# Kernel optimization log

Measured on AMD Instinct MI355X. Metric: run time of the kernel, lower is better.

## Reference

```python
import jax, jax.numpy as jnp
import numpy as np
import math

B, C, L = 16, 2048, 64

def setup_inputs() -> dict:
    key = jax.random.key(0)
    kq, kk, kv = jax.random.split(key, 3)
    q = jax.random.normal(kq, (B, C, L), dtype=jnp.float32)
    k = jax.random.normal(kk, (B, C, L), dtype=jnp.float32)
    v = jax.random.normal(kv, (B, C, L), dtype=jnp.float32)
    return {"q": q, "k": k, "v": v}

def reference(q, k, v):
    b, c, l = q.shape
    # Faithful to the torch source: k is RESHAPED (row-major), not transposed.
    k_t = k.reshape(b, l, c)                      # (b, l, c)
    score = jnp.matmul(q, k_t) / math.sqrt(l)     # (b, c, c)
    # nn.Softmax() with no dim on a 3D tensor -> torch implicit dim = 0 (batch axis)
    score = jax.nn.softmax(score, axis=0)
    return jnp.matmul(score, v)                   # (b, c, l)
```

## Files before the change

kernel.cpp:

```cpp
#include <hip/hip_runtime.h>

typedef __attribute__((ext_vector_type(8))) short short8;
typedef __attribute__((ext_vector_type(4))) float float4v;

#define BATCH 16
#define CDIM 2048
#define LDIM 64
#define BSTRIDE (CDIM * LDIM)

#if __has_builtin(__builtin_amdgcn_exp2f)
#define EXPW(x) __builtin_amdgcn_exp2f(x)
#define QSCALE 0.18033688011112042f
#else
#define EXPW(x) __expf(x)
#define QSCALE 0.125f
#endif

#define WAITV(n) asm volatile("s_waitcnt vmcnt(" #n ")" ::: "memory")
#define BARRIER() asm volatile("s_barrier" ::: "memory")

__device__ __forceinline__ float bf2f(unsigned short u) {
    return __uint_as_float(((unsigned int)u) << 16);
}
__device__ __forceinline__ unsigned short f2bf(float f) {
    unsigned int x = __float_as_uint(f);
    x += 0x7fffu + ((x >> 16) & 1u);
    return (unsigned short)(x >> 16);
}
#if __has_builtin(__builtin_amdgcn_cvt_pk_bf16_f32)
__device__ __forceinline__ unsigned int pk2bf(float a, float b) {
    auto t = __builtin_amdgcn_cvt_pk_bf16_f32(a, b);
    unsigned int u;
    __builtin_memcpy(&u, &t, 4);
    return u;
}
#else
__device__ __forceinline__ unsigned int pk2bf(float a, float b) {
    return f2bf(a) | ((unsigned)f2bf(b) << 16);
}
#endif
__device__ __forceinline__ void dma16(const void* g, void* l) {
    __builtin_amdgcn_global_load_lds(
        (const __attribute__((address_space(1))) void*)g,
        (__attribute__((address_space(3))) void*)l, 16, 0, 0);
}

__global__ __launch_bounds__(256) void prepass_kernel(
    const float* __restrict__ q, const float* __restrict__ k,
    unsigned short* __restrict__ qb, unsigned short* __restrict__ kT)
{
    __shared__ float T[64][68];
    const int bx = blockIdx.x;
    const int t = threadIdx.x;

    if (bx < 1024) {
        int i = bx * 256 + t;
        const float4v* src = (const float4v*)q + (size_t)i * 2;
        float4v x0 = src[0], x1 = src[1];
        unsigned int u0 = pk2bf(x0[0] * QSCALE, x0[1] * QSCALE);
        unsigned int u1 = pk2bf(x0[2] * QSCALE, x0[3] * QSCALE);
        unsigned int u2 = pk2bf(x1[0] * QSCALE, x1[1] * QSCALE);
        unsigned int u3 = pk2bf(x1[2] * QSCALE, x1[3] * QSCALE);
        int b = i >> 14, r = i & 16383, m = r >> 3, j = r & 7;
        *(uint4*)(qb + (size_t)b * BSTRIDE + m * 64 + (j ^ (m & 7)) * 8) =
            make_uint4(u0, u1, u2, u3);
    } else {
        int idx = bx - 1024, b = idx >> 5, n0 = (idx & 31) * 64;
        const float* src = k + (size_t)b * BSTRIDE + (size_t)(t >> 2) * 2048 + n0 + (t & 3) * 16;
#pragma unroll
        for (int kk = 0; kk < 4; kk++) {
            float4v x = *(const float4v*)(src + kk * 4);
#pragma unroll
            for (int e = 0; e < 4; e++)
                T[t >> 2][(t & 3) * 16 + kk * 4 + e] = x[e];
        }
        __syncthreads();
        unsigned short* dst = kT + (size_t)b * BSTRIDE;
        int n = t & 63;
#pragma unroll
        for (int jj = 0; jj < 2; jj++) {
            int j = (t >> 6) * 2 + jj;
            *(uint4*)(dst + (size_t)(n0 + n) * 64 + (j ^ (n & 7)) * 8) =
                make_uint4(pk2bf(T[j * 8 + 0][n], T[j * 8 + 1][n]),
                           pk2bf(T[j * 8 + 2][n], T[j * 8 + 3][n]),
                           pk2bf(T[j * 8 + 4][n], T[j * 8 + 5][n]),
                           pk2bf(T[j * 8 + 6][n], T[j * 8 + 7][n]));
        }
    }
}

__global__ __launch_bounds__(256, 3) void dinv_vpre_kernel(
    const unsigned short* __restrict__ qb, const unsigned short* __restrict__ kT,
    const float* __restrict__ v, unsigned short* __restrict__ vS,
    unsigned short* __restrict__ Dt)
{
    __shared__ __align__(16) unsigned char smem[24576];

    const int tid = threadIdx.x;

    if (blockIdx.x >= 512) {
        float (*T)[68] = (float(*)[68])smem;
#pragma unroll 1
        for (int tt = 0; tt < 2; tt++) {
            int idx = (blockIdx.x - 512) * 2 + tt, b = idx >> 5, n0 = (idx & 31) * 64;
            const float* src = v + (size_t)b * BSTRIDE + (size_t)n0 * 64 +
                               (size_t)(tid >> 2) * 64 + (tid & 3) * 16;
#pragma unroll
            for (int kk = 0; kk < 4; kk++) {
                float4v x = *(const float4v*)(src + kk * 4);
#pragma unroll
                for (int e = 0; e < 4; e++)
                    T[tid >> 2][(tid & 3) * 16 + kk * 4 + e] = x[e];
            }
            __syncthreads();
            unsigned short* dst = vS + (size_t)b * BSTRIDE;
            int j = tid & 63, qc = tid >> 6;
            int sw = qc ^ (j & 3) ^ ((j >> 2) & 3);
#pragma unroll
            for (int nb = 0; nb < 2; nb++) {
                *(uint4*)(dst + (size_t)(n0 / 32 + nb) * 2048 + j * 32 + sw * 8) =
                    make_uint4(pk2bf(T[nb * 32 + qc * 8 + 0][j], T[nb * 32 + qc * 8 + 1][j]),
                               pk2bf(T[nb * 32 + qc * 8 + 2][j], T[nb * 32 + qc * 8 + 3][j]),
                               pk2bf(T[nb * 32 + qc * 8 + 4][j], T[nb * 32 + qc * 8 + 5][j]),
                               pk2bf(T[nb * 32 + qc * 8 + 6][j], T[nb * 32 + qc * 8 + 7][j]));
            }
            __syncthreads();
        }
        return;
    }

    const int w = tid >> 6, lane = tid & 63;
    const int c = lane & 15, q = lane >> 4;
    const int xcd = blockIdx.x & 7, slot = blockIdx.x >> 3;
    const int mtB = xcd * 2 + (slot >> 5), ng = slot & 31;
    const int m0 = mtB * 128, n0 = ng * 64;

    float4v Dacc[2][4];
#pragma unroll
    for (int ms = 0; ms < 2; ms++)
#pragma unroll
        for (int nt = 0; nt < 4; nt++) Dacc[ms][nt] = (float4v){0.f, 0.f, 0.f, 0.f};

    const char* qrow0 = (const char*)qb + (size_t)(m0 + w * 32 + c) * 128;
    short8 Qf[2][2], Qn[2][2];
#pragma unroll
    for (int ms = 0; ms < 2; ms++)
#pragma unroll
        for (int h = 0; h < 2; h++)
            Qf[ms][h] = *(const short8*)(qrow0 + ms * 16 * 128 + ((h * 4 + q) ^ (c & 7)) * 16);

    {
        const char* kg0 = (const char*)(kT + (size_t)n0 * 64);
        const char* kg1 = (const char*)(kT + (size_t)BSTRIDE + (size_t)n0 * 64);
        dma16(kg0 + (w * 2 + 0) * 1024 + lane * 16, (char*)smem + (w * 2 + 0) * 1024);
        dma16(kg0 + (w * 2 + 1) * 1024 + lane * 16, (char*)smem + (w * 2 + 1) * 1024);
        dma16(kg1 + (w * 2 + 0) * 1024 + lane * 16, (char*)smem + 8192 + (w * 2 + 0) * 1024);
        dma16(kg1 + (w * 2 + 1) * 1024 + lane * 16, (char*)smem + 8192 + (w * 2 + 1) * 1024);
    }

    int cur = 0, pre = 2;
    for (int bb = 0; bb < BATCH; bb++) {
        if (bb == 0) { WAITV(2); }
        else if (bb == 15) { WAITV(4); }
        else { WAITV(6); }
        BARRIER();

        if (bb < BATCH - 1) {
            const char* qn = qrow0 + (size_t)(bb + 1) * (BSTRIDE * 2);
#pragma unroll
            for (int ms = 0; ms < 2; ms++)
#pragma unroll
                for (int h = 0; h < 2; h++)
                    Qn[ms][h] = *(const short8*)(qn + ms * 16 * 128 + ((h * 4 + q) ^ (c & 7)) * 16);
        }
        if (bb < BATCH - 2) {
            const char* kg = (const char*)(kT + (size_t)(bb + 2) * BSTRIDE + (size_t)n0 * 64);
            dma16(kg + (w * 2 + 0) * 1024 + lane * 16,
                  (char*)smem + pre * 8192 + (w * 2 + 0) * 1024);
            dma16(kg + (w * 2 + 1) * 1024 + lane * 16,
                  (char*)smem + pre * 8192 + (w * 2 + 1) * 1024);
        }
        const char* sk = (const char*)smem + cur * 8192;
        __builtin_amdgcn_s_setprio(1);
#pragma unroll
        for (int nt = 0; nt < 4; nt++) {
            short8 A0 = *(const short8*)(sk + (nt * 16 + c) * 128 + ((q) ^ (c & 7)) * 16);
            short8 A1 = *(const short8*)(sk + (nt * 16 + c) * 128 + ((4 + q) ^ (c & 7)) * 16);
#pragma unroll
            for (int ms = 0; ms < 2; ms++) {
                float4v d = (float4v){0.f, 0.f, 0.f, 0.f};
                d = __builtin_amdgcn_mfma_f32_16x16x32_bf16(A0, Qf[ms][0], d, 0, 0, 0);
                d = __builtin_amdgcn_mfma_f32_16x16x32_bf16(A1, Qf[ms][1], d, 0, 0, 0);
#pragma unroll
                for (int r = 0; r < 4; r++) Dacc[ms][nt][r] += EXPW(d[r]);
            }
        }
        __builtin_amdgcn_s_setprio(0);
        if (bb < BATCH - 1) {
#pragma unroll
            for (int ms = 0; ms < 2; ms++)
#pragma unroll
                for (int h = 0; h < 2; h++)
                    Qf[ms][h] = Qn[ms][h];
        }
        cur = (cur == 2) ? 0 : cur + 1;
        pre = (pre == 2) ? 0 : pre + 1;
    }

#pragma unroll
    for (int ms = 0; ms < 2; ms++)
#pragma unroll
        for (int nt = 0; nt < 4; nt++) {
            unsigned int x = pk2bf(__builtin_amdgcn_rcpf(Dacc[ms][nt][0]),
                                   __builtin_amdgcn_rcpf(Dacc[ms][nt][1]));
            unsigned int y = pk2bf(__builtin_amdgcn_rcpf(Dacc[ms][nt][2]),
                                   __builtin_amdgcn_rcpf(Dacc[ms][nt][3]));
            size_t tm = (size_t)(mtB * 8 + w * 2 + ms);
            size_t tp = (size_t)(ng * 2 + (nt >> 1));
            *(uint2*)((char*)Dt + (tm * 64 + tp) * 1024 + c * 64 + q * 16 + (nt & 1) * 8) =
                make_uint2(x, y);
        }
}

__global__ __launch_bounds__(512, 4) void attn_main_kernel(
    const unsigned short* __restrict__ qb, const unsigned short* __restrict__ kT,
    const unsigned short* __restrict__ vS, const unsigned short* __restrict__ Dt,
    float* __restrict__ out)
{
    __shared__ __align__(16) unsigned char smem[49152];

    const int tid = threadIdx.x, w = tid >> 6, lane = tid & 63;
    const int c = lane & 15, q = lane >> 4;
    const int g = w >> 2, ns = w & 3;
    const int xcd = blockIdx.x & 7, slot = blockIdx.x >> 3;
    const int b = slot & 15, mt = xcd * 4 + (slot >> 4);
    const int m0 = mt * 64;
    const int nbase = ns * 512;

    const unsigned short* qb_b = qb + (size_t)b * BSTRIDE;
    const char* kbase = (const char*)(kT + (size_t)b * BSTRIDE);
    const char* vbase = (const char*)(vS + (size_t)b * BSTRIDE);
    char* skb = (char*)smem + ns * 12288;

    short8 Qf[2][2];
#pragma unroll
    for (int ms = 0; ms < 2; ms++)
#pragma unroll
        for (int h = 0; h < 2; h++)
            Qf[ms][h] = *(const short8*)(qb_b + (m0 + g * 32 + ms * 16 + c) * 64 +
                                         ((h * 4 + q) ^ (c & 7)) * 8);
    float4v acc[2][4];
#pragma unroll
    for (int ms = 0; ms < 2; ms++)
#pragma unroll
        for (int jt = 0; jt < 4; jt++) acc[ms][jt] = (float4v){0.f, 0.f, 0.f, 0.f};

    const char* dtw0 = (const char*)Dt +
        ((size_t)(mt * 4 + g * 2 + 0) * 64 + ns * 16) * 1024 + c * 64 + q * 16;
    const char* dtw1 = dtw0 + (size_t)64 * 1024;

    const int vsw = (q ^ (c & 3) ^ ((c >> 2) & 3)) * 16;

    dma16(kbase + (size_t)nbase * 128 + (2 * g + 0) * 1024 + lane * 16, skb + (2 * g + 0) * 1024);
    dma16(kbase + (size_t)nbase * 128 + (2 * g + 1) * 1024 + lane * 16, skb + (2 * g + 1) * 1024);
    dma16(kbase + (size_t)(nbase + 32) * 128 + (2 * g + 0) * 1024 + lane * 16,
          skb + 4096 + (2 * g + 0) * 1024);
    dma16(kbase + (size_t)(nbase + 32) * 128 + (2 * g + 1) * 1024 + lane * 16,
          skb + 4096 + (2 * g + 1) * 1024);
    uint4 du[2];
    du[0] = *(const uint4*)(dtw0);
    du[1] = *(const uint4*)(dtw1);

    int cur = 0, pre = 2;
    for (int st = 0; st < 16; st++) {
        if (st == 0) { WAITV(4); }
        else if (st == 15) { WAITV(0); }
        else { WAITV(8); }
        BARRIER();

        uint4 nu[2] = {du[0], du[1]};
        if (st < 15) {
            nu[0] = *(const uint4*)(dtw0 + (size_t)(st + 1) * 1024);
            nu[1] = *(const uint4*)(dtw1 + (size_t)(st + 1) * 1024);
        }
        short8 Vr[4];
        {
            const char* vtile = vbase + (size_t)(ns * 16 + st) * 4096;
#pragma unroll
            for (int jt = 0; jt < 4; jt++)
                Vr[jt] = *(const short8*)(vtile + (jt * 16 + c) * 64 + vsw);
        }
        if (st < 14) {
            const int n2 = nbase + (st + 2) * 32;
            dma16(kbase + (size_t)n2 * 128 + (2 * g + 0) * 1024 + lane * 16,
                  skb + pre * 4096 + (2 * g + 0) * 1024);
            dma16(kbase + (size_t)n2 * 128 + (2 * g + 1) * 1024 + lane * 16,
                  skb + pre * 4096 + (2 * g + 1) * 1024);
        }

        const char* skp = skb + cur * 4096;
        unsigned int pr[2][2][2];
        __builtin_amdgcn_s_setprio(1);
#pragma unroll
        for (int nt = 0; nt < 2; nt++) {
            short8 A0 = *(const short8*)(skp + (nt * 16 + c) * 128 + ((q) ^ (c & 7)) * 16);
            short8 A1 = *(const short8*)(skp + (nt * 16 + c) * 128 + ((4 + q) ^ (c & 7)) * 16);
#pragma unroll
            for (int ms = 0; ms < 2; ms++) {
                float4v d = (float4v){0.f, 0.f, 0.f, 0.f};
                d = __builtin_amdgcn_mfma_f32_16x16x32_bf16(A0, Qf[ms][0], d, 0, 0, 0);
                d = __builtin_amdgcn_mfma_f32_16x16x32_bf16(A1, Qf[ms][1], d, 0, 0, 0);
                unsigned int ux = nt ? du[ms].z : du[ms].x;
                unsigned int uy = nt ? du[ms].w : du[ms].y;
                pr[ms][nt][0] = pk2bf(EXPW(d[0]) * __uint_as_float(ux << 16),
                                      EXPW(d[1]) * __uint_as_float(ux & 0xffff0000u));
                pr[ms][nt][1] = pk2bf(EXPW(d[2]) * __uint_as_float(uy << 16),
                                      EXPW(d[3]) * __uint_as_float(uy & 0xffff0000u));
            }
        }
        __builtin_amdgcn_s_setprio(0);

        union PU { unsigned int i[4]; short8 s; };
        PU pu0, pu1;
#if __has_builtin(__builtin_amdgcn_permlane32_swap) && __has_builtin(__builtin_amdgcn_permlane16_swap)
        {
            typedef __attribute__((ext_vector_type(2))) unsigned int uint2v;
            uint2v ab, cd;
            ab = __builtin_amdgcn_permlane32_swap(pr[0][0][0], pr[0][1][0], false, false);
            cd = __builtin_amdgcn_permlane16_swap(ab.x, ab.y, false, false);
            pu0.i[0] = cd.x; pu0.i[2] = cd.y;
            ab = __builtin_amdgcn_permlane32_swap(pr[0][0][1], pr[0][1][1], false, false);
            cd = __builtin_amdgcn_permlane16_swap(ab.x, ab.y, false, false);
            pu0.i[1] = cd.x; pu0.i[3] = cd.y;
            ab = __builtin_amdgcn_permlane32_swap(pr[1][0][0], pr[1][1][0], false, false);
            cd = __builtin_amdgcn_permlane16_swap(ab.x, ab.y, false, false);
            pu1.i[0] = cd.x; pu1.i[2] = cd.y;
            ab = __builtin_amdgcn_permlane32_swap(pr[1][0][1], pr[1][1][1], false, false);
            cd = __builtin_amdgcn_permlane16_swap(ab.x, ab.y, false, false);
            pu1.i[1] = cd.x; pu1.i[3] = cd.y;
        }
#else
#pragma unroll
        for (int t = 0; t < 4; t++) {
            int src = (2 * (q & 1) + (t >> 1)) * 16 + c;
            int a0 = __shfl((int)pr[0][0][t & 1], src);
            int b0 = __shfl((int)pr[0][1][t & 1], src);
            pu0.i[t] = (unsigned int)((q >= 2) ? b0 : a0);
            int a1 = __shfl((int)pr[1][0][t & 1], src);
            int b1 = __shfl((int)pr[1][1][t & 1], src);
            pu1.i[t] = (unsigned int)((q >= 2) ? b1 : a1);
        }
#endif

        __builtin_amdgcn_s_setprio(1);
#pragma unroll
        for (int jt = 0; jt < 4; jt++) {
            acc[0][jt] = __builtin_amdgcn_mfma_f32_16x16x32_bf16(pu0.s, Vr[jt], acc[0][jt], 0, 0, 0);
            acc[1][jt] = __builtin_amdgcn_mfma_f32_16x16x32_bf16(pu1.s, Vr[jt], acc[1][jt], 0, 0, 0);
        }
        __builtin_amdgcn_s_setprio(0);
        du[0] = nu[0]; du[1] = nu[1];
        cur = (cur == 2) ? 0 : cur + 1;
        pre = (pre == 2) ? 0 : pre + 1;
    }

    __syncthreads();
    {
        float* cpy = (float*)((char*)smem + (ns & 1) * 17408);
        if (ns < 2) {
#pragma unroll
            for (int ms = 0; ms < 2; ms++)
#pragma unroll
                for (int jt = 0; jt < 4; jt++)
#pragma unroll
                    for (int r = 0; r < 4; r++)
                        cpy[(g * 32 + ms * 16 + q * 4 + r) * 68 + jt * 16 + c] = acc[ms][jt][r];
        }
    }
    __syncthreads();
    {
        float* cpy = (float*)((char*)smem + (ns & 1) * 17408);
        if (ns >= 2) {
#pragma unroll
            for (int ms = 0; ms < 2; ms++)
#pragma unroll
                for (int jt = 0; jt < 4; jt++)
#pragma unroll
                    for (int r = 0; r < 4; r++)
                        cpy[(g * 32 + ms * 16 + q * 4 + r) * 68 + jt * 16 + c] += acc[ms][jt][r];
        }
    }
    __syncthreads();
    {
        int ml = tid >> 3, j0 = (tid & 7) * 8;
        const float* c0 = (const float*)smem + ml * 68 + j0;
        const float* c1 = (const float*)((char*)smem + 17408) + ml * 68 + j0;
        float4v s0 = *(const float4v*)c0 + *(const float4v*)c1;
        float4v s1 = *(const float4v*)(c0 + 4) + *(const float4v*)(c1 + 4);
        float* dst = out + ((size_t)b * CDIM + m0 + ml) * LDIM + j0;
        *(float4v*)dst = s0;
        *(float4v*)(dst + 4) = s1;
    }
}

extern "C" void kernel_launch(void* const* d_in, const int* in_sizes, int n_in,
                              void* d_out, int out_size, void* d_ws, size_t ws_size,
                              hipStream_t stream) {
    const float* q = (const float*)d_in[0];
    const float* k = (const float*)d_in[1];
    const float* v = (const float*)d_in[2];
    float* out = (float*)d_out;

    unsigned short* qb = (unsigned short*)d_ws;
    unsigned short* kT = qb + (size_t)BATCH * BSTRIDE;
    unsigned short* vS = kT + (size_t)BATCH * BSTRIDE;
    unsigned short* Dt = vS + (size_t)BATCH * BSTRIDE;

    prepass_kernel<<<1536, 256, 0, stream>>>(q, k, qb, kT);
    dinv_vpre_kernel<<<768, 256, 0, stream>>>(qb, kT, v, vS, Dt);
    attn_main_kernel<<<512, 512, 0, stream>>>(qb, kT, vS, Dt, out);
}
```

Baseline: 118.6 us.

## Load K tiles directly from global into registers, dropping LDS staging and barriers

The triple-buffered async copy of K tiles into shared memory, with its per-iteration vmcnt waits and s_barrier, is replaced by direct swizzled global loads of K fragments into registers for each wave. This removes block-wide synchronisation from the main loop and cuts shared memory from 48 KB to 34 KB, which may allow more resident blocks per CU. The cost is that the two wave groups sharing a K strip now each fetch it from cache rather than sharing one LDS copy. The K loads are also issued in the same iteration they are used, with no prefetch distance, so their latency may be exposed.

```diff
diff --git a/kernel.cpp b/kernel.cpp
--- a/kernel.cpp
+++ b/kernel.cpp
@@ -227,7 +227,7 @@
     const unsigned short* __restrict__ vS, const unsigned short* __restrict__ Dt,
     float* __restrict__ out)
 {
-    __shared__ __align__(16) unsigned char smem[49152];
+    __shared__ __align__(16) unsigned char smem[34816];
 
     const int tid = threadIdx.x, w = tid >> 6, lane = tid & 63;
     const int c = lane & 15, q = lane >> 4;
@@ -240,7 +240,6 @@
     const unsigned short* qb_b = qb + (size_t)b * BSTRIDE;
     const char* kbase = (const char*)(kT + (size_t)b * BSTRIDE);
     const char* vbase = (const char*)(vS + (size_t)b * BSTRIDE);
-    char* skb = (char*)smem + ns * 12288;
 
     short8 Qf[2][2];
 #pragma unroll
@@ -260,24 +259,16 @@
     const char* dtw1 = dtw0 + (size_t)64 * 1024;
 
     const int vsw = (q ^ (c & 3) ^ ((c >> 2) & 3)) * 16;
-
-    dma16(kbase + (size_t)nbase * 128 + (2 * g + 0) * 1024 + lane * 16, skb + (2 * g + 0) * 1024);
-    dma16(kbase + (size_t)nbase * 128 + (2 * g + 1) * 1024 + lane * 16, skb + (2 * g + 1) * 1024);
-    dma16(kbase + (size_t)(nbase + 32) * 128 + (2 * g + 0) * 1024 + lane * 16,
-          skb + 4096 + (2 * g + 0) * 1024);
-    dma16(kbase + (size_t)(nbase + 32) * 128 + (2 * g + 1) * 1024 + lane * 16,
-          skb + 4096 + (2 * g + 1) * 1024);
+    const int ksw0 = ((q) ^ (c & 7)) * 16;
+    const int ksw1 = ((4 + q) ^ (c & 7)) * 16;
+
     uint4 du[2];
     du[0] = *(const uint4*)(dtw0);
     du[1] = *(const uint4*)(dtw1);
 
-    int cur = 0, pre = 2;
+    const char* kstrip = kbase + (size_t)nbase * 128;
+
     for (int st = 0; st < 16; st++) {
-        if (st == 0) { WAITV(4); }
-        else if (st == 15) { WAITV(0); }
-        else { WAITV(8); }
-        BARRIER();
-
         uint4 nu[2] = {du[0], du[1]};
         if (st < 15) {
             nu[0] = *(const uint4*)(dtw0 + (size_t)(st + 1) * 1024);
@@ -290,26 +281,23 @@
             for (int jt = 0; jt < 4; jt++)
                 Vr[jt] = *(const short8*)(vtile + (jt * 16 + c) * 64 + vsw);
         }
-        if (st < 14) {
-            const int n2 = nbase + (st + 2) * 32;
-            dma16(kbase + (size_t)n2 * 128 + (2 * g + 0) * 1024 + lane * 16,
-                  skb + pre * 4096 + (2 * g + 0) * 1024);
-            dma16(kbase + (size_t)n2 * 128 + (2 * g + 1) * 1024 + lane * 16,
-                  skb + pre * 4096 + (2 * g + 1) * 1024);
-        }
-
-        const char* skp = skb + cur * 4096;
+        const char* ktile = kstrip + (size_t)st * 4096;
+        short8 KA0[2], KA1[2];
+#pragma unroll
+        for (int nt = 0; nt < 2; nt++) {
+            KA0[nt] = *(const short8*)(ktile + (nt * 16 + c) * 128 + ksw0);
+            KA1[nt] = *(const short8*)(ktile + (nt * 16 + c) * 128 + ksw1);
+        }
+
         unsigned int pr[2][2][2];
         __builtin_amdgcn_s_setprio(1);
 #pragma unroll
         for (int nt = 0; nt < 2; nt++) {
-            short8 A0 = *(const short8*)(skp + (nt * 16 + c) * 128 + ((q) ^ (c & 7)) * 16);
-            short8 A1 = *(const short8*)(skp + (nt * 16 + c) * 128 + ((4 + q) ^ (c & 7)) * 16);
 #pragma unroll
             for (int ms = 0; ms < 2; ms++) {
                 float4v d = (float4v){0.f, 0.f, 0.f, 0.f};
-                d = __builtin_amdgcn_mfma_f32_16x16x32_bf16(A0, Qf[ms][0], d, 0, 0, 0);
-                d = __builtin_amdgcn_mfma_f32_16x16x32_bf16(A1, Qf[ms][1], d, 0, 0, 0);
+                d = __builtin_amdgcn_mfma_f32_16x16x32_bf16(KA0[nt], Qf[ms][0], d, 0, 0, 0);
+                d = __builtin_amdgcn_mfma_f32_16x16x32_bf16(KA1[nt], Qf[ms][1], d, 0, 0, 0);
                 unsigned int ux = nt ? du[ms].z : du[ms].x;
                 unsigned int uy = nt ? du[ms].w : du[ms].y;
                 pr[ms][nt][0] = pk2bf(EXPW(d[0]) * __uint_as_float(ux << 16),
@@ -360,11 +348,8 @@
         }
         __builtin_amdgcn_s_setprio(0);
         du[0] = nu[0]; du[1] = nu[1];
-        cur = (cur == 2) ? 0 : cur + 1;
-        pre = (pre == 2) ? 0 : pre + 1;
-    }
-
-    __syncthreads();
+    }
+
     {
         float* cpy = (float*)((char*)smem + (ns & 1) * 17408);
         if (ns < 2) {
```

New measurement: 125.0 us. +5.4%, slower.
